# Kernel tuning notes

Measured on AMD Instinct MI355X. Metric: run time of the kernel, lower is better.

The kernel has to match this reference:

```python
import jax, jax.numpy as jnp
import numpy as np

T, B, D, H = 1024, 256, 32, 128


def setup_inputs() -> dict:
    key = jax.random.key(0)
    k1, k2, k3, k4, k5 = jax.random.split(key, 5)
    return {
        "x": jax.random.normal(k1, (T, B, D), dtype=jnp.float32),
        "state": jax.random.normal(k2, (B, H), dtype=jnp.float32),
        "W_in": jax.random.normal(k3, (D, H), dtype=jnp.float32) * 0.1,
        "W_h": jax.random.normal(k4, (H, H), dtype=jnp.float32) * 0.1,
        "b": jax.random.normal(k5, (H,), dtype=jnp.float32) * 0.1,
    }


def reference(x, state, W_in, W_h, b):
    # DifferenceEqLayer: loop the cell over time dim 0, stacking outputs.
    # Cell (explicit Euler step): h' = h + tanh(x_t @ W_in + h @ W_h + b); out = h'.
    def step(h, x_t):
        h_new = h + jnp.tanh(x_t @ W_in + h @ W_h + b)  # [B, H]
        return h_new, h_new

    final_state, outputs = jax.lax.scan(step, state, x)  # outputs: [T, B, H]
    return outputs, final_state
```

## Files before the change

### kernel.cpp

```cpp
#include <hip/hip_runtime.h>
#include <math.h>

#define T_DIM 1024
#define B_DIM 256
#define D_DIM 32
#define H_DIM 128

__device__ __forceinline__ float xla_tanh_fma_f32(float x) {
  const float plim = 7.99881172180175781f;
  float xc = fminf(fmaxf(x, -plim), plim);
  float x2 = __fmul_rn(xc, xc);
  float p;
  p = fmaf(x2, -2.76076847742355e-16f, 2.00018790482477e-13f);
  p = fmaf(x2, p, -8.60467152213735e-11f);
  p = fmaf(x2, p,  5.12229709037114e-08f);
  p = fmaf(x2, p,  1.48572235717979e-05f);
  p = fmaf(x2, p,  6.37261928875436e-04f);
  p = fmaf(x2, p,  4.89352455891786e-03f);
  float num = __fmul_rn(xc, p);
  float q;
  q = fmaf(x2, 1.19825839466702e-06f, 1.18534705686654e-04f);
  q = fmaf(x2, q, 2.26843463243900e-03f);
  q = fmaf(x2, q, 4.89352518554385e-03f);
  float r = __fdiv_rn(num, q);
  return (fabsf(x) < 0.0004f) ? x : r;
}

__device__ __forceinline__ float dpp_shr1(float v) {
  return __int_as_float(__builtin_amdgcn_update_dpp(
      __float_as_int(v), __float_as_int(v), 0x111, 0xf, 0xf, false));
}

__global__ __launch_bounds__(256, 1) void diffeq_kernel(
    const float* __restrict__ x, const float* __restrict__ state,
    const float* __restrict__ W_in, const float* __restrict__ W_h,
    const float* __restrict__ bias, float* __restrict__ out) {
  __shared__ __align__(16) float h0[H_DIM];
  __shared__ __align__(16) float h1[H_DIM];

  const int b   = blockIdx.x;
  const int tid = threadIdx.x;
  const int p   = tid >> 1;
  const int i   = tid & 1;

  float wh[64];
#pragma unroll
  for (int m = 0; m < 64; ++m) wh[m] = W_h[(64 * i + m) * H_DIM + p];
  float wx[16];
#pragma unroll
  for (int m = 0; m < 16; ++m) wx[m] = W_in[(16 * i + m) * H_DIM + p];
  const float bj = bias[p];
  float hown = state[(size_t)b * H_DIM + p];

  if (tid < H_DIM) h0[tid] = state[(size_t)b * H_DIM + tid];

  const size_t out_row = (size_t)b * H_DIM + p;
  const float4* xg4 = reinterpret_cast<const float4*>(x + (size_t)b * D_DIM);
  const int xs4 = B_DIM * D_DIM / 4;
  __syncthreads();

#define STEP(HRD, HWR, TIDX) { \
    const float4* hb4 = reinterpret_cast<const float4*>(HRD); \
    const float4* xr4 = xg4 + (size_t)(TIDX) * xs4 + 4 * i; \
    float4 xq0 = xr4[0], xq1 = xr4[1], xq2 = xr4[2], xq3 = xr4[3]; \
    float s1 = 0.f, s2 = 0.f; \
    _Pragma("unroll") \
    for (int r = 0; r < 2; ++r) { \
      _Pragma("unroll") \
      for (int m = 0; m < 16; ++m) { \
        float4 h4 = hb4[16 * i + m]; \
        s2 = fmaf(h4.x, wh[4 * m + 0], s2); \
        s2 = fmaf(h4.y, wh[4 * m + 1], s2); \
        s2 = fmaf(h4.z, wh[4 * m + 2], s2); \
        s2 = fmaf(h4.w, wh[4 * m + 3], s2); \
      } \
      s1 = fmaf(xq0.x, wx[0],  s1); s1 = fmaf(xq0.y, wx[1],  s1); \
      s1 = fmaf(xq0.z, wx[2],  s1); s1 = fmaf(xq0.w, wx[3],  s1); \
      s1 = fmaf(xq1.x, wx[4],  s1); s1 = fmaf(xq1.y, wx[5],  s1); \
      s1 = fmaf(xq1.z, wx[6],  s1); s1 = fmaf(xq1.w, wx[7],  s1); \
      s1 = fmaf(xq2.x, wx[8],  s1); s1 = fmaf(xq2.y, wx[9],  s1); \
      s1 = fmaf(xq2.z, wx[10], s1); s1 = fmaf(xq2.w, wx[11], s1); \
      s1 = fmaf(xq3.x, wx[12], s1); s1 = fmaf(xq3.y, wx[13], s1); \
      s1 = fmaf(xq3.z, wx[14], s1); s1 = fmaf(xq3.w, wx[15], s1); \
      if (r < 1) { s1 = dpp_shr1(s1); s2 = dpp_shr1(s2); } \
    } \
    float a  = __fadd_rn(__fadd_rn(s1, s2), bj); \
    float th = xla_tanh_fma_f32(a); \
    float hv = __fadd_rn(hown, th); \
    if (i == 1) (HWR)[p] = hv; \
    hown = hv;   \
    __syncthreads(); \
    if (i == 1) out[(size_t)(TIDX) * (B_DIM * H_DIM) + out_row] = hv; \
  }

  for (int t = 0; t < T_DIM; t += 2) {
    STEP(h0, h1, t)
    STEP(h1, h0, t + 1)
  }

  if (i == 1) out[(size_t)T_DIM * B_DIM * H_DIM + out_row] = hown;
}

extern "C" void kernel_launch(void* const* d_in, const int* in_sizes, int n_in,
                              void* d_out, int out_size, void* d_ws, size_t ws_size,
                              hipStream_t stream) {
  const float* x     = (const float*)d_in[0];
  const float* state = (const float*)d_in[1];
  const float* W_in  = (const float*)d_in[2];
  const float* W_h   = (const float*)d_in[3];
  const float* bias  = (const float*)d_in[4];
  float* out = (float*)d_out;

  diffeq_kernel<<<B_DIM, 256, 0, stream>>>(x, state, W_in, W_h, bias, out);
}
```

Before: 683.1 us.

## Prefetch next-step x rows into registers and pad shared h halves

Loads the x inputs for the next timestep one step ahead into registers, so the global load latency overlaps the current step's recurrence math instead of sitting on the serial critical path. It also pads the shared hidden-state buffer so the two thread halves read from offset banks (stride 68 floats), which should cut LDS bank conflicts on the float4 broadcast reads. The cost is extra registers for the double-buffered x values, on a kernel that already holds 80 weight values per thread, plus one redundant load on the final iteration.

```diff
diff --git a/kernel.cpp b/kernel.cpp
--- a/kernel.cpp
+++ b/kernel.cpp
@@ -5,6 +5,7 @@
 #define B_DIM 256
 #define D_DIM 32
 #define H_DIM 128
+#define HP 68
 
 __device__ __forceinline__ float xla_tanh_fma_f32(float x) {
   const float plim = 7.99881172180175781f;
@@ -35,8 +36,8 @@
     const float* __restrict__ x, const float* __restrict__ state,
     const float* __restrict__ W_in, const float* __restrict__ W_h,
     const float* __restrict__ bias, float* __restrict__ out) {
-  __shared__ __align__(16) float h0[H_DIM];
-  __shared__ __align__(16) float h1[H_DIM];
+  __shared__ __align__(16) float h0[2 * HP];
+  __shared__ __align__(16) float h1[2 * HP];
 
   const int b   = blockIdx.x;
   const int tid = threadIdx.x;
@@ -52,50 +53,64 @@
   const float bj = bias[p];
   float hown = state[(size_t)b * H_DIM + p];
 
-  if (tid < H_DIM) h0[tid] = state[(size_t)b * H_DIM + tid];
+  if (tid < H_DIM)
+    h0[HP * (tid >> 6) + (tid & 63)] = state[(size_t)b * H_DIM + tid];
 
   const size_t out_row = (size_t)b * H_DIM + p;
   const float4* xg4 = reinterpret_cast<const float4*>(x + (size_t)b * D_DIM);
   const int xs4 = B_DIM * D_DIM / 4;
+
+  float4 xa0, xa1, xa2, xa3, xb0, xb1, xb2, xb3;
+  {
+    const float4* xp = xg4 + 4 * i;
+    xa0 = xp[0]; xa1 = xp[1]; xa2 = xp[2]; xa3 = xp[3];
+  }
   __syncthreads();
 
-#define STEP(HRD, HWR, TIDX) { \
+#define STEP(HRD, HWR, X0, X1, X2, X3, TIDX) { \
     const float4* hb4 = reinterpret_cast<const float4*>(HRD); \
-    const float4* xr4 = xg4 + (size_t)(TIDX) * xs4 + 4 * i; \
-    float4 xq0 = xr4[0], xq1 = xr4[1], xq2 = xr4[2], xq3 = xr4[3]; \
     float s1 = 0.f, s2 = 0.f; \
     _Pragma("unroll") \
     for (int r = 0; r < 2; ++r) { \
       _Pragma("unroll") \
       for (int m = 0; m < 16; ++m) { \
-        float4 h4 = hb4[16 * i + m]; \
+        float4 h4 = hb4[17 * i + m];      \
         s2 = fmaf(h4.x, wh[4 * m + 0], s2); \
         s2 = fmaf(h4.y, wh[4 * m + 1], s2); \
         s2 = fmaf(h4.z, wh[4 * m + 2], s2); \
         s2 = fmaf(h4.w, wh[4 * m + 3], s2); \
       } \
-      s1 = fmaf(xq0.x, wx[0],  s1); s1 = fmaf(xq0.y, wx[1],  s1); \
-      s1 = fmaf(xq0.z, wx[2],  s1); s1 = fmaf(xq0.w, wx[3],  s1); \
-      s1 = fmaf(xq1.x, wx[4],  s1); s1 = fmaf(xq1.y, wx[5],  s1); \
-      s1 = fmaf(xq1.z, wx[6],  s1); s1 = fmaf(xq1.w, wx[7],  s1); \
-      s1 = fmaf(xq2.x, wx[8],  s1); s1 = fmaf(xq2.y, wx[9],  s1); \
-      s1 = fmaf(xq2.z, wx[10], s1); s1 = fmaf(xq2.w, wx[11], s1); \
-      s1 = fmaf(xq3.x, wx[12], s1); s1 = fmaf(xq3.y, wx[13], s1); \
-      s1 = fmaf(xq3.z, wx[14], s1); s1 = fmaf(xq3.w, wx[15], s1); \
+      s1 = fmaf(X0.x, wx[0],  s1); s1 = fmaf(X0.y, wx[1],  s1); \
+      s1 = fmaf(X0.z, wx[2],  s1); s1 = fmaf(X0.w, wx[3],  s1); \
+      s1 = fmaf(X1.x, wx[4],  s1); s1 = fmaf(X1.y, wx[5],  s1); \
+      s1 = fmaf(X1.z, wx[6],  s1); s1 = fmaf(X1.w, wx[7],  s1); \
+      s1 = fmaf(X2.x, wx[8],  s1); s1 = fmaf(X2.y, wx[9],  s1); \
+      s1 = fmaf(X2.z, wx[10], s1); s1 = fmaf(X2.w, wx[11], s1); \
+      s1 = fmaf(X3.x, wx[12], s1); s1 = fmaf(X3.y, wx[13], s1); \
+      s1 = fmaf(X3.z, wx[14], s1); s1 = fmaf(X3.w, wx[15], s1); \
       if (r < 1) { s1 = dpp_shr1(s1); s2 = dpp_shr1(s2); } \
     } \
     float a  = __fadd_rn(__fadd_rn(s1, s2), bj); \
     float th = xla_tanh_fma_f32(a); \
     float hv = __fadd_rn(hown, th); \
-    if (i == 1) (HWR)[p] = hv; \
+    if (i == 1) (HWR)[HP * (p >> 6) + (p & 63)] = hv; \
     hown = hv;   \
     __syncthreads(); \
     if (i == 1) out[(size_t)(TIDX) * (B_DIM * H_DIM) + out_row] = hv; \
   }
 
   for (int t = 0; t < T_DIM; t += 2) {
-    STEP(h0, h1, t)
-    STEP(h1, h0, t + 1)
+    {
+      const float4* xp = xg4 + (size_t)(t + 1) * xs4 + 4 * i;
+      xb0 = xp[0]; xb1 = xp[1]; xb2 = xp[2]; xb3 = xp[3];
+    }
+    STEP(h0, h1, xa0, xa1, xa2, xa3, t)
+    {
+      int t2 = (t + 2 < T_DIM) ? (t + 2) : (T_DIM - 1);
+      const float4* xp = xg4 + (size_t)t2 * xs4 + 4 * i;
+      xa0 = xp[0]; xa1 = xp[1]; xa2 = xp[2]; xa3 = xp[3];
+    }
+    STEP(h1, h0, xb0, xb1, xb2, xb3, t + 1)
   }
 
   if (i == 1) out[(size_t)T_DIM * B_DIM * H_DIM + out_row] = hown;
```

Result: faster. 652.3 us (-4.5%).

## Use one thread per hidden unit with weights split across registers and LDS

Applied to the files above, without the earlier changes.

Each hidden unit is now computed by a single thread in 128-thread blocks, instead of being split across two threads that were combined with a DPP shift. The first 32 rows of W_h stay in registers, while the remaining 96 rows and all of W_in move to shared memory. This removes the cross-lane reduction and halves the wave count per barrier. In exchange, each thread runs a serial chain of 160 FMAs per step, two-thirds of its weights come from LDS, and the serial dependency per timestep gets longer.

```diff
diff --git a/kernel.cpp b/kernel.cpp
--- a/kernel.cpp
+++ b/kernel.cpp
@@ -26,71 +26,85 @@
   return (fabsf(x) < 0.0004f) ? x : r;
 }
 
-__device__ __forceinline__ float dpp_shr1(float v) {
-  return __int_as_float(__builtin_amdgcn_update_dpp(
-      __float_as_int(v), __float_as_int(v), 0x111, 0xf, 0xf, false));
-}
-
-__global__ __launch_bounds__(256, 1) void diffeq_kernel(
+__global__ __launch_bounds__(128, 1) void diffeq_kernel(
     const float* __restrict__ x, const float* __restrict__ state,
     const float* __restrict__ W_in, const float* __restrict__ W_h,
     const float* __restrict__ bias, float* __restrict__ out) {
+  __shared__ float WHH[96 * H_DIM];
+  __shared__ float WI[D_DIM * H_DIM];
   __shared__ __align__(16) float h0[H_DIM];
   __shared__ __align__(16) float h1[H_DIM];
 
-  const int b   = blockIdx.x;
-  const int tid = threadIdx.x;
-  const int p   = tid >> 1;
-  const int i   = tid & 1;
+  const int b = blockIdx.x;
+  const int j = threadIdx.x;
 
-  float wh[64];
+  for (int r = 0; r < 96; ++r) WHH[r * H_DIM + j] = W_h[(32 + r) * H_DIM + j];
 #pragma unroll
-  for (int m = 0; m < 64; ++m) wh[m] = W_h[(64 * i + m) * H_DIM + p];
-  float wx[16];
+  for (int r = 0; r < D_DIM; ++r) WI[r * H_DIM + j] = W_in[r * H_DIM + j];
+
+  float whlo[32];
 #pragma unroll
-  for (int m = 0; m < 16; ++m) wx[m] = W_in[(16 * i + m) * H_DIM + p];
-  const float bj = bias[p];
-  float hown = state[(size_t)b * H_DIM + p];
+  for (int k = 0; k < 32; ++k) whlo[k] = W_h[k * H_DIM + j];
+  const float bj = bias[j];
 
-  if (tid < H_DIM) h0[tid] = state[(size_t)b * H_DIM + tid];
+  float hown = state[(size_t)b * H_DIM + j];
+  h0[j] = hown;
+  __syncthreads();
 
-  const size_t out_row = (size_t)b * H_DIM + p;
+  const size_t out_row = (size_t)b * H_DIM + j;
   const float4* xg4 = reinterpret_cast<const float4*>(x + (size_t)b * D_DIM);
   const int xs4 = B_DIM * D_DIM / 4;
-  __syncthreads();
 
 #define STEP(HRD, HWR, TIDX) { \
-    const float4* hb4 = reinterpret_cast<const float4*>(HRD); \
-    const float4* xr4 = xg4 + (size_t)(TIDX) * xs4 + 4 * i; \
-    float4 xq0 = xr4[0], xq1 = xr4[1], xq2 = xr4[2], xq3 = xr4[3]; \
-    float s1 = 0.f, s2 = 0.f; \
+     \
+    const float4* xp = xg4 + (size_t)(TIDX) * xs4; \
+    float4 x0 = xp[0], x1 = xp[1], x2_ = xp[2], x3 = xp[3]; \
+    float4 x4 = xp[4], x5 = xp[5], x6 = xp[6], x7 = xp[7]; \
+    const float4* hq4 = reinterpret_cast<const float4*>(HRD); \
+     \
+    float s2 = 0.f; \
     _Pragma("unroll") \
-    for (int r = 0; r < 2; ++r) { \
-      _Pragma("unroll") \
-      for (int m = 0; m < 16; ++m) { \
-        float4 h4 = hb4[16 * i + m]; \
-        s2 = fmaf(h4.x, wh[4 * m + 0], s2); \
-        s2 = fmaf(h4.y, wh[4 * m + 1], s2); \
-        s2 = fmaf(h4.z, wh[4 * m + 2], s2); \
-        s2 = fmaf(h4.w, wh[4 * m + 3], s2); \
-      } \
-      s1 = fmaf(xq0.x, wx[0],  s1); s1 = fmaf(xq0.y, wx[1],  s1); \
-      s1 = fmaf(xq0.z, wx[2],  s1); s1 = fmaf(xq0.w, wx[3],  s1); \
-      s1 = fmaf(xq1.x, wx[4],  s1); s1 = fmaf(xq1.y, wx[5],  s1); \
-      s1 = fmaf(xq1.z, wx[6],  s1); s1 = fmaf(xq1.w, wx[7],  s1); \
-      s1 = fmaf(xq2.x, wx[8],  s1); s1 = fmaf(xq2.y, wx[9],  s1); \
-      s1 = fmaf(xq2.z, wx[10], s1); s1 = fmaf(xq2.w, wx[11], s1); \
-      s1 = fmaf(xq3.x, wx[12], s1); s1 = fmaf(xq3.y, wx[13], s1); \
-      s1 = fmaf(xq3.z, wx[14], s1); s1 = fmaf(xq3.w, wx[15], s1); \
-      if (r < 1) { s1 = dpp_shr1(s1); s2 = dpp_shr1(s2); } \
+    for (int q = 0; q < 8; ++q) { \
+      float4 h4 = hq4[q];                        \
+      s2 = fmaf(h4.x, whlo[4 * q + 0], s2); \
+      s2 = fmaf(h4.y, whlo[4 * q + 1], s2); \
+      s2 = fmaf(h4.z, whlo[4 * q + 2], s2); \
+      s2 = fmaf(h4.w, whlo[4 * q + 3], s2); \
     } \
+    _Pragma("unroll") \
+    for (int q = 8; q < 32; ++q) { \
+      float4 h4 = hq4[q];                        \
+      s2 = fmaf(h4.x, WHH[(4 * q - 32 + 0) * H_DIM + j], s2); \
+      s2 = fmaf(h4.y, WHH[(4 * q - 32 + 1) * H_DIM + j], s2); \
+      s2 = fmaf(h4.z, WHH[(4 * q - 32 + 2) * H_DIM + j], s2); \
+      s2 = fmaf(h4.w, WHH[(4 * q - 32 + 3) * H_DIM + j], s2); \
+    } \
+     \
+    float s1 = 0.f; \
+    s1 = fmaf(x0.x, WI[0  * H_DIM + j], s1); s1 = fmaf(x0.y, WI[1  * H_DIM + j], s1); \
+    s1 = fmaf(x0.z, WI[2  * H_DIM + j], s1); s1 = fmaf(x0.w, WI[3  * H_DIM + j], s1); \
+    s1 = fmaf(x1.x, WI[4  * H_DIM + j], s1); s1 = fmaf(x1.y, WI[5  * H_DIM + j], s1); \
+    s1 = fmaf(x1.z, WI[6  * H_DIM + j], s1); s1 = fmaf(x1.w, WI[7  * H_DIM + j], s1); \
+    s1 = fmaf(x2_.x, WI[8 * H_DIM + j], s1); s1 = fmaf(x2_.y, WI[9  * H_DIM + j], s1); \
+    s1 = fmaf(x2_.z, WI[10 * H_DIM + j], s1); s1 = fmaf(x2_.w, WI[11 * H_DIM + j], s1); \
+    s1 = fmaf(x3.x, WI[12 * H_DIM + j], s1); s1 = fmaf(x3.y, WI[13 * H_DIM + j], s1); \
+    s1 = fmaf(x3.z, WI[14 * H_DIM + j], s1); s1 = fmaf(x3.w, WI[15 * H_DIM + j], s1); \
+    s1 = fmaf(x4.x, WI[16 * H_DIM + j], s1); s1 = fmaf(x4.y, WI[17 * H_DIM + j], s1); \
+    s1 = fmaf(x4.z, WI[18 * H_DIM + j], s1); s1 = fmaf(x4.w, WI[19 * H_DIM + j], s1); \
+    s1 = fmaf(x5.x, WI[20 * H_DIM + j], s1); s1 = fmaf(x5.y, WI[21 * H_DIM + j], s1); \
+    s1 = fmaf(x5.z, WI[22 * H_DIM + j], s1); s1 = fmaf(x5.w, WI[23 * H_DIM + j], s1); \
+    s1 = fmaf(x6.x, WI[24 * H_DIM + j], s1); s1 = fmaf(x6.y, WI[25 * H_DIM + j], s1); \
+    s1 = fmaf(x6.z, WI[26 * H_DIM + j], s1); s1 = fmaf(x6.w, WI[27 * H_DIM + j], s1); \
+    s1 = fmaf(x7.x, WI[28 * H_DIM + j], s1); s1 = fmaf(x7.y, WI[29 * H_DIM + j], s1); \
+    s1 = fmaf(x7.z, WI[30 * H_DIM + j], s1); s1 = fmaf(x7.w, WI[31 * H_DIM + j], s1); \
     float a  = __fadd_rn(__fadd_rn(s1, s2), bj); \
     float th = xla_tanh_fma_f32(a); \
     float hv = __fadd_rn(hown, th); \
-    if (i == 1) (HWR)[p] = hv; \
-    hown = hv;   \
+    (HWR)[j] = hv; \
+    hown = hv; \
     __syncthreads(); \
-    if (i == 1) out[(size_t)(TIDX) * (B_DIM * H_DIM) + out_row] = hv; \
+     \
+    out[(size_t)(TIDX) * (B_DIM * H_DIM) + out_row] = hv; \
   }
 
   for (int t = 0; t < T_DIM; t += 2) {
@@ -98,7 +112,7 @@
     STEP(h1, h0, t + 1)
   }
 
-  if (i == 1) out[(size_t)T_DIM * B_DIM * H_DIM + out_row] = hown;
+  out[(size_t)T_DIM * B_DIM * H_DIM + out_row] = hown;
 }
 
 extern "C" void kernel_launch(void* const* d_in, const int* in_sizes, int n_in,
@@ -111,5 +125,5 @@
   const float* bias  = (const float*)d_in[4];
   float* out = (float*)d_out;
 
-  diffeq_kernel<<<B_DIM, 256, 0, stream>>>(x, state, W_in, W_h, bias, out);
+  diffeq_kernel<<<B_DIM, 128, 0, stream>>>(x, state, W_in, W_h, bias, out);
 }
```

New measurement: 2.408 ms. +252.5%, slower.
